# Kernel optimization log

Hardware: AMD Instinct MI355X
Metric: run time of the kernel (lower is better)

## Reference

```python
import jax, jax.numpy as jnp
import numpy as np

B, S, T, C, H = 16, 64, 4096, 512, 8
D = C // H
NEG = jnp.float32(-1e30)


def setup_inputs() -> dict:
    key = jax.random.key(0)
    ks = jax.random.split(key, 12)
    x = jax.random.normal(ks[0], (1, C, 1), dtype=jnp.float32)
    eh = jax.random.normal(ks[1], (B, C, T), dtype=jnp.float32)
    # ragged shot boundaries -> fixed (B, S) start/end arrays, end > start
    bounds = jnp.sort(jax.random.randint(ks[2], (B, S + 1), 0, T), axis=-1)
    shot_starts = bounds[:, :-1].astype(jnp.int32)
    shot_ends = jnp.maximum(bounds[:, 1:], shot_starts + 1).astype(jnp.int32)
    sc = 1.0 / np.sqrt(C)
    Wq = jax.random.normal(ks[3], (C, C), dtype=jnp.float32) * sc
    bq = jnp.zeros((C,), dtype=jnp.float32)
    Wk = jax.random.normal(ks[4], (C, C), dtype=jnp.float32) * sc
    bk = jnp.zeros((C,), dtype=jnp.float32)
    Wv = jax.random.normal(ks[5], (C, C), dtype=jnp.float32) * sc
    bv = jnp.zeros((C,), dtype=jnp.float32)
    Wp = jax.random.normal(ks[6], (C, C), dtype=jnp.float32) * sc
    bp = jnp.zeros((C,), dtype=jnp.float32)
    return {"x": x, "encoder_hidden_states": eh, "shot_starts": shot_starts,
            "shot_ends": shot_ends, "Wq": Wq, "bq": bq, "Wk": Wk, "bk": bk,
            "Wv": Wv, "bv": bv, "Wp": Wp, "bp": bp}


def reference(x, encoder_hidden_states, shot_starts, shot_ends,
              Wq, bq, Wk, bk, Wv, bv, Wp, bp):
    scale = 1.0 / np.sqrt(D)
    # 1x1 conv == pointwise matmul over channels
    q = (Wq @ x[0] + bq[:, None])            # (C, 1)
    k = jnp.einsum('oc,bct->bot', Wk, encoder_hidden_states) + bk[None, :, None]
    v = jnp.einsum('oc,bct->bot', Wv, encoder_hidden_states) + bv[None, :, None]
    qh = q.reshape(H, D) * scale             # (H, D) single query per head
    kh = k.reshape(B, H, D, T)               # (B, H, D, T)
    vh = v.reshape(B, H, D, T).transpose(0, 1, 3, 2)  # (B, H, T, D)
    att = jnp.einsum('hd,bhdt->bht', qh, kh)          # (B, H, T)
    pos = jnp.arange(T)
    seg = (pos[None, None, :] >= shot_starts[:, :, None]) & \
          (pos[None, None, :] < shot_ends[:, :, None])  # (B, S, T)
    logits = jnp.where(seg[:, :, None, :], att[:, None, :, :], NEG)  # (B,S,H,T)
    p = jax.nn.softmax(logits, axis=-1)
    out = jnp.einsum('bsht,bhtd->bshd', p, vh)        # (B, S, H, D)
    out = out.reshape(B * S, C)
    out = out @ Wp.T + bp                              # proj (1x1 conv)
    return out[:, :, None]                             # (B*S, C, 1)
```

## Files before the change

### kernel.cpp

```cpp
#include <hip/hip_runtime.h>
#include <cstdint>
#include <cstddef>

#define B_ 16
#define S_ 64
#define T_ 4096
#define C_ 512
#define H_ 8

#define WS_QKT     0
#define WS_QB      4096
#define WS_QH      4104
#define WS_MS      4616
#define WS_LI      12808
#define WS_CNT     21000
#define WS_CSEG    21016
#define WS_CIDX    23064
#define WS_CMUL    25112
#define WS_ATT     28672
#define WS_WSUM    552960
#define WS_ATTNOUT 4747264

__global__ void k_prep1(const float* __restrict__ x, const float* __restrict__ Wq,
                        const float* __restrict__ bq, float* __restrict__ qh_g) {
  __shared__ float xs[C_];
  __shared__ float red[256];
  int tid = threadIdx.x;
  xs[tid] = x[tid];
  xs[tid + 256] = x[tid + 256];
  __syncthreads();
  int r0 = blockIdx.x * 32;
  int rl = tid >> 3, sub = tid & 7;
  int r = r0 + rl;
  const float* wr = Wq + (size_t)r * C_ + sub * 64;
  const float* xp = xs + sub * 64;
  float s = 0.f;
#pragma unroll
  for (int i = 0; i < 64; i += 4) {
    float4 w = *(const float4*)(wr + i);
    s += w.x * xp[i] + w.y * xp[i + 1] + w.z * xp[i + 2] + w.w * xp[i + 3];
  }
  red[tid] = s;
  __syncthreads();
  if (sub == 0) {
    float tot = bq[r];
#pragma unroll
    for (int i = 0; i < 8; ++i) tot += red[rl * 8 + i];
    qh_g[r] = tot * 0.125f;
  }
}

__global__ void k_prep2(const float* __restrict__ qh_g,
                        const float* __restrict__ Wk,
                        const float* __restrict__ bk, float* __restrict__ qkT,
                        float* __restrict__ qb) {
  __shared__ float qhs[64];
  int tid = threadIdx.x;
  int h = blockIdx.x;
  if (tid < 64) qhs[tid] = qh_g[h * 64 + tid];
  __syncthreads();
  int c0 = tid, c1 = tid + 256;
  float s0 = 0.f, s1 = 0.f;
#pragma unroll 8
  for (int d = 0; d < 64; ++d) {
    const float* row = Wk + (size_t)(h * 64 + d) * C_;
    float q = qhs[d];
    s0 += q * row[c0];
    s1 += q * row[c1];
  }
  qkT[c0 * 8 + h] = s0;
  qkT[c1 * 8 + h] = s1;
  if (tid < 64) {
    float w = qhs[tid] * bk[h * 64 + tid];
#pragma unroll
    for (int off = 32; off > 0; off >>= 1) w += __shfl_down(w, off, 64);
    if (tid == 0) qb[h] = w;
  }
}

__global__ __launch_bounds__(256, 4) void k_att(
    const float* __restrict__ eh, const float* __restrict__ qkT,
    const float* __restrict__ qb, float* __restrict__ att) {
  __shared__ float qks[C_ * 8];
  __shared__ float part[4 * 8 * 64];
  int tid = threadIdx.x;
  int tl = tid & 63, cg = tid >> 6;
  int b = blockIdx.y;
  int t0 = blockIdx.x * 64;
#pragma unroll
  for (int i = 0; i < 16; ++i) qks[tid + i * 256] = qkT[tid + i * 256];
  __syncthreads();
  const float* ehp = eh + ((size_t)b * C_ + (size_t)cg * 128) * T_ + t0 + tl;
  float acc[8];
#pragma unroll
  for (int h = 0; h < 8; ++h) acc[h] = 0.f;
#pragma unroll 4
  for (int j = 0; j < 128; ++j) {
    float e = ehp[(size_t)j * T_];
    const float4 q0 = *(const float4*)&qks[(cg * 128 + j) * 8];
    const float4 q1 = *(const float4*)&qks[(cg * 128 + j) * 8 + 4];
    acc[0] += q0.x * e; acc[1] += q0.y * e; acc[2] += q0.z * e; acc[3] += q0.w * e;
    acc[4] += q1.x * e; acc[5] += q1.y * e; acc[6] += q1.z * e; acc[7] += q1.w * e;
  }
#pragma unroll
  for (int h = 0; h < 8; ++h) part[(cg * 8 + h) * 64 + tl] = acc[h];
  __syncthreads();
#pragma unroll
  for (int i = 0; i < 2; ++i) {
    int idx = tid + i * 256;
    int h = idx >> 6, tt = idx & 63;
    float v = part[(0 * 8 + h) * 64 + tt] + part[(1 * 8 + h) * 64 + tt] +
              part[(2 * 8 + h) * 64 + tt] + part[(3 * 8 + h) * 64 + tt] + qb[h];
    att[((size_t)b * H_ + h) * T_ + t0 + tt] = v;
  }
}

__global__ void k_stats(const float* __restrict__ att,
                        const int* __restrict__ starts,
                        const int* __restrict__ ends, float* __restrict__ ms,
                        float* __restrict__ li) {
  int tid = threadIdx.x;
  int n = blockIdx.x;
  int b = n >> 6;
  int start = starts[n], end = ends[n];
  int h = tid >> 5, tl = tid & 31;
  const float* ah = att + ((size_t)b * H_ + h) * T_;
  float mloc = -3.0e38f;
  for (int t = start + tl; t < end; t += 32) mloc = fmaxf(mloc, ah[t]);
#pragma unroll
  for (int off = 16; off > 0; off >>= 1)
    mloc = fmaxf(mloc, __shfl_xor(mloc, off, 32));
  float lloc = 0.f;
  for (int t = start + tl; t < end; t += 32) lloc += __expf(ah[t] - mloc);
#pragma unroll
  for (int off = 16; off > 0; off >>= 1) lloc += __shfl_xor(lloc, off, 32);
  if (tl == 0) { ms[n * 8 + h] = mloc; li[n * 8 + h] = 1.f / lloc; }
}

__global__ void k_map(const int* __restrict__ starts,
                      const int* __restrict__ ends, int* __restrict__ cnt,
                      int* __restrict__ cseg, int* __restrict__ cidx,
                      int* __restrict__ cmul) {
  __shared__ int sc[1024];
  int n = threadIdx.x;
  int st = starts[n], en = ends[n];
  int cbase = st & ~31;
  int nch = (en - cbase + 127) >> 7;
  sc[n] = nch;
  __syncthreads();
  for (int off = 1; off < 1024; off <<= 1) {
    int v = 0;
    if (n >= off) v = sc[n - off];
    __syncthreads();
    sc[n] += v;
    __syncthreads();
  }
  int pre = sc[n] - nch;
  for (int k = 0; k < nch; ++k) {
    cseg[pre + k] = n;
    cidx[pre + k] = k;
    cmul[pre + k] = (nch > 1) ? 1 : 0;
  }
  if (n == 1023) cnt[0] = sc[n];
}

__global__ __launch_bounds__(256, 4) void k_wsum(
    const float* __restrict__ eh, const float* __restrict__ att,
    const float* __restrict__ ms, const float* __restrict__ li,
    const int* __restrict__ starts, const int* __restrict__ ends,
    const int* __restrict__ cnt, const int* __restrict__ cseg,
    const int* __restrict__ cidx, const int* __restrict__ cmul,
    float* __restrict__ wsum) {
  __shared__ float pl[8 * 136];
  int i = blockIdx.x;
  if (i >= cnt[0]) return;
  int tid = threadIdx.x;
  int n = cseg[i];
  int k = cidx[i];
  int mul = cmul[i];
  int b = n >> 6;
  int st = starts[n], en = ends[n];
  int cbase = st & ~31;
  int t_lo = cbase + k * 128;
  if (st > t_lo) t_lo = st;
  int t_hi = cbase + (k + 1) * 128;
  if (en < t_hi) t_hi = en;
  int base = t_lo & ~3;

  int h = tid >> 5, l32 = tid & 31;
  float msn = ms[n * 8 + h], lin = li[n * 8 + h];
  const float* ah = att + ((size_t)b * H_ + h) * T_;
  for (int j = l32; j < 136; j += 32) {
    int t = base + j;
    float pv = 0.f;
    if (t >= t_lo && t < t_hi) pv = __expf(ah[t] - msn) * lin;
    pl[h * 136 + j] = pv;
  }
  __syncthreads();

  float acc0[8], acc1[8];
#pragma unroll
  for (int hh = 0; hh < 8; ++hh) { acc0[hh] = 0.f; acc1[hh] = 0.f; }
  const float* e0p = eh + ((size_t)b * C_ + tid) * T_ + base;
  const float* e1p = e0p + (size_t)256 * T_;
  int jmax = t_hi - base;
  int jv = jmax & ~3;
#pragma unroll 4
  for (int j = 0; j < jv; j += 4) {
    float4 e0 = *(const float4*)(e0p + j);
    float4 e1 = *(const float4*)(e1p + j);
#pragma unroll
    for (int hh = 0; hh < 8; ++hh) {
      const float4 p = *(const float4*)&pl[hh * 136 + j];
      acc0[hh] += p.x * e0.x + p.y * e0.y + p.z * e0.z + p.w * e0.w;
      acc1[hh] += p.x * e1.x + p.y * e1.y + p.z * e1.z + p.w * e1.w;
    }
  }
  for (int j = jv; j < jmax; ++j) {
    float e0 = e0p[j], e1 = e1p[j];
#pragma unroll
    for (int hh = 0; hh < 8; ++hh) {
      float p = pl[hh * 136 + j];
      acc0[hh] += p * e0;
      acc1[hh] += p * e1;
    }
  }
  float* wp = wsum + (size_t)n * (H_ * C_);
  if (!mul) {
#pragma unroll
    for (int hh = 0; hh < 8; ++hh) {
      wp[hh * C_ + tid] = acc0[hh];
      wp[hh * C_ + 256 + tid] = acc1[hh];
    }
  } else {
#pragma unroll
    for (int hh = 0; hh < 8; ++hh) {
      atomicAdd(&wp[hh * C_ + tid], acc0[hh]);
      atomicAdd(&wp[hh * C_ + 256 + tid], acc1[hh]);
    }
  }
}

__global__ __launch_bounds__(256, 4) void k_gemm(
    const float* __restrict__ A, long aRow, long aColPerY,
    const float* __restrict__ Bm, const float* __restrict__ bias,
    float* __restrict__ Cc) {
  __shared__ float As[32 * 36];
  __shared__ float Bs[64 * 36];
  int tid = threadIdx.x;
  int n0 = blockIdx.x * 32;
  int y = blockIdx.y;
  const float* Abase = A + (size_t)n0 * aRow + (size_t)y * aColPerY;
  const float* Bbase = Bm + (size_t)(y * 64) * C_;
  int tx = tid & 15, ty = tid >> 4;
  float acc[2][4];
#pragma unroll
  for (int a = 0; a < 2; ++a)
#pragma unroll
    for (int bb = 0; bb < 4; ++bb) acc[a][bb] = 0.f;
  for (int k0 = 0; k0 < 512; k0 += 32) {
#pragma unroll
    for (int i = 0; i < 4; ++i) {
      int idx = tid + i * 256;
      int r = idx >> 5, cc = idx & 31;
      As[r * 36 + cc] = Abase[(size_t)r * aRow + k0 + cc];
    }
#pragma unroll
    for (int i = 0; i < 8; ++i) {
      int idx = tid + i * 256;
      int r = idx >> 5, cc = idx & 31;
      Bs[r * 36 + cc] = Bbase[(size_t)r * C_ + k0 + cc];
    }
    __syncthreads();
#pragma unroll
    for (int k = 0; k < 32; k += 4) {
      const float4 a0 = *(const float4*)&As[(ty * 2 + 0) * 36 + k];
      const float4 a1 = *(const float4*)&As[(ty * 2 + 1) * 36 + k];
#pragma unroll
      for (int bb = 0; bb < 4; ++bb) {
        const float4 bv = *(const float4*)&Bs[(tx * 4 + bb) * 36 + k];
        acc[0][bb] += a0.x * bv.x + a0.y * bv.y + a0.z * bv.z + a0.w * bv.w;
        acc[1][bb] += a1.x * bv.x + a1.y * bv.y + a1.z * bv.z + a1.w * bv.w;
      }
    }
    __syncthreads();
  }
#pragma unroll
  for (int a = 0; a < 2; ++a) {
    int nn = n0 + ty * 2 + a;
    float4 o;
    o.x = acc[a][0] + bias[y * 64 + tx * 4 + 0];
    o.y = acc[a][1] + bias[y * 64 + tx * 4 + 1];
    o.z = acc[a][2] + bias[y * 64 + tx * 4 + 2];
    o.w = acc[a][3] + bias[y * 64 + tx * 4 + 3];
    *(float4*)&Cc[(size_t)nn * C_ + y * 64 + tx * 4] = o;
  }
}

extern "C" void kernel_launch(void* const* d_in, const int* in_sizes, int n_in,
                              void* d_out, int out_size, void* d_ws,
                              size_t ws_size, hipStream_t stream) {
  const float* x = (const float*)d_in[0];
  const float* eh = (const float*)d_in[1];
  const int* shot_starts = (const int*)d_in[2];
  const int* shot_ends = (const int*)d_in[3];
  const float* Wq = (const float*)d_in[4];
  const float* bq = (const float*)d_in[5];
  const float* Wk = (const float*)d_in[6];
  const float* bk = (const float*)d_in[7];
  const float* Wv = (const float*)d_in[8];
  const float* bv = (const float*)d_in[9];
  const float* Wp = (const float*)d_in[10];
  const float* bp = (const float*)d_in[11];
  float* out = (float*)d_out;

  float* ws = (float*)d_ws;
  float* qkT = ws + WS_QKT;
  float* qb = ws + WS_QB;
  float* qh = ws + WS_QH;
  float* ms = ws + WS_MS;
  float* li = ws + WS_LI;
  int* cnt = (int*)(ws + WS_CNT);
  int* cseg = (int*)(ws + WS_CSEG);
  int* cidx = (int*)(ws + WS_CIDX);
  int* cmul = (int*)(ws + WS_CMUL);
  float* att = ws + WS_ATT;
  float* wsum = ws + WS_WSUM;
  float* attnout = ws + WS_ATTNOUT;

  hipMemsetAsync(wsum, 0, (size_t)1024 * H_ * C_ * sizeof(float), stream);
  k_prep1<<<16, 256, 0, stream>>>(x, Wq, bq, qh);
  k_prep2<<<8, 256, 0, stream>>>(qh, Wk, bk, qkT, qb);
  k_att<<<dim3(T_ / 64, B_), 256, 0, stream>>>(eh, qkT, qb, att);
  k_stats<<<B_ * S_, 256, 0, stream>>>(att, shot_starts, shot_ends, ms, li);
  k_map<<<1, 1024, 0, stream>>>(shot_starts, shot_ends, cnt, cseg, cidx, cmul);
  k_wsum<<<2048, 256, 0, stream>>>(eh, att, ms, li, shot_starts, shot_ends,
                                   cnt, cseg, cidx, cmul, wsum);
  k_gemm<<<dim3(32, 8), 256, 0, stream>>>(wsum, (long)(H_ * C_), (long)C_, Wv,
                                          bv, attnout);
  k_gemm<<<dim3(32, 8), 256, 0, stream>>>(attnout, (long)C_, 0L, Wp, bp, out);
}
```

Baseline: 367.4 us.

## Restructure weighted-sum kernel so lane groups cover contiguous time chunks per channel

The weighted-sum kernel used to give each thread one channel pair and walk time serially, so every lane read a different row with a large stride. Now each group of 4 lanes shares a channel and reads 64 contiguous bytes of time per step. Partial sums are combined with shuffles, and the kernel makes 8 passes over 64 channels. Chunk alignment moves from 32 to 16 elements to cut wasted work at segment edges. The cost is extra shuffle reductions, loads clamped near the end of the row, and more passes per block.

Measured after the change: 347.4 us. 1.06x faster.

```diff
diff --git a/kernel.cpp b/kernel.cpp
--- a/kernel.cpp
+++ b/kernel.cpp
@@ -144,7 +144,7 @@
   __shared__ int sc[1024];
   int n = threadIdx.x;
   int st = starts[n], en = ends[n];
-  int cbase = st & ~31;
+  int cbase = st & ~15;
   int nch = (en - cbase + 127) >> 7;
   sc[n] = nch;
   __syncthreads();
@@ -180,63 +180,78 @@
   int mul = cmul[i];
   int b = n >> 6;
   int st = starts[n], en = ends[n];
-  int cbase = st & ~31;
-  int t_lo = cbase + k * 128;
-  if (st > t_lo) t_lo = st;
-  int t_hi = cbase + (k + 1) * 128;
+  int cbase = st & ~15;
+  int base = cbase + (k << 7);
+  int t_lo = (st > base) ? st : base;
+  int t_hi = base + 128;
   if (en < t_hi) t_hi = en;
-  int base = t_lo & ~3;
-
-  int h = tid >> 5, l32 = tid & 31;
-  float msn = ms[n * 8 + h], lin = li[n * 8 + h];
-  const float* ah = att + ((size_t)b * H_ + h) * T_;
-  for (int j = l32; j < 136; j += 32) {
-    int t = base + j;
-    float pv = 0.f;
-    if (t >= t_lo && t < t_hi) pv = __expf(ah[t] - msn) * lin;
-    pl[h * 136 + j] = pv;
-  }
-  __syncthreads();
-
-  float acc0[8], acc1[8];
-#pragma unroll
-  for (int hh = 0; hh < 8; ++hh) { acc0[hh] = 0.f; acc1[hh] = 0.f; }
-  const float* e0p = eh + ((size_t)b * C_ + tid) * T_ + base;
-  const float* e1p = e0p + (size_t)256 * T_;
   int jmax = t_hi - base;
-  int jv = jmax & ~3;
-#pragma unroll 4
-  for (int j = 0; j < jv; j += 4) {
-    float4 e0 = *(const float4*)(e0p + j);
-    float4 e1 = *(const float4*)(e1p + j);
-#pragma unroll
-    for (int hh = 0; hh < 8; ++hh) {
-      const float4 p = *(const float4*)&pl[hh * 136 + j];
-      acc0[hh] += p.x * e0.x + p.y * e0.y + p.z * e0.z + p.w * e0.w;
-      acc1[hh] += p.x * e1.x + p.y * e1.y + p.z * e1.z + p.w * e1.w;
-    }
-  }
-  for (int j = jv; j < jmax; ++j) {
-    float e0 = e0p[j], e1 = e1p[j];
-#pragma unroll
-    for (int hh = 0; hh < 8; ++hh) {
-      float p = pl[hh * 136 + j];
-      acc0[hh] += p * e0;
-      acc1[hh] += p * e1;
-    }
-  }
+  int kmax = (jmax + 15) >> 4;
+
+  {
+    int h = tid >> 5, l32 = tid & 31;
+    float msn = ms[n * 8 + h], lin = li[n * 8 + h];
+    const float* ah = att + ((size_t)b * H_ + h) * T_;
+    for (int j = l32; j < 136; j += 32) {
+      int t = base + j;
+      float pv = 0.f;
+      if (t >= t_lo && t < t_hi) pv = __expf(ah[t] - msn) * lin;
+      pl[h * 136 + j] = pv;
+    }
+  }
+  __syncthreads();
+
+  int l = tid & 63, wv = tid >> 6;
+  int il = l & 3, g = l >> 2;
   float* wp = wsum + (size_t)n * (H_ * C_);
-  if (!mul) {
-#pragma unroll
-    for (int hh = 0; hh < 8; ++hh) {
-      wp[hh * C_ + tid] = acc0[hh];
-      wp[hh * C_ + 256 + tid] = acc1[hh];
-    }
-  } else {
-#pragma unroll
-    for (int hh = 0; hh < 8; ++hh) {
-      atomicAdd(&wp[hh * C_ + tid], acc0[hh]);
-      atomicAdd(&wp[hh * C_ + 256 + tid], acc1[hh]);
+
+  for (int pass = 0; pass < 8; ++pass) {
+    int ch = pass * 64 + wv * 16 + g;
+    const float* erow = eh + ((size_t)b * C_ + ch) * T_;
+    float a0 = 0.f, a1 = 0.f, a2 = 0.f, a3 = 0.f;
+    float a4 = 0.f, a5 = 0.f, a6 = 0.f, a7 = 0.f;
+#pragma unroll 2
+    for (int kk = 0; kk < kmax; ++kk) {
+      int j0 = (kk << 4) | (il << 2);
+      int tg = base + j0;
+      if (tg > T_ - 4) tg = T_ - 4;
+      float4 ev = *(const float4*)(erow + tg);
+      const float* pp = pl + j0;
+      float4 p;
+      p = *(const float4*)(pp + 0 * 136);
+      a0 += p.x * ev.x + p.y * ev.y + p.z * ev.z + p.w * ev.w;
+      p = *(const float4*)(pp + 1 * 136);
+      a1 += p.x * ev.x + p.y * ev.y + p.z * ev.z + p.w * ev.w;
+      p = *(const float4*)(pp + 2 * 136);
+      a2 += p.x * ev.x + p.y * ev.y + p.z * ev.z + p.w * ev.w;
+      p = *(const float4*)(pp + 3 * 136);
+      a3 += p.x * ev.x + p.y * ev.y + p.z * ev.z + p.w * ev.w;
+      p = *(const float4*)(pp + 4 * 136);
+      a4 += p.x * ev.x + p.y * ev.y + p.z * ev.z + p.w * ev.w;
+      p = *(const float4*)(pp + 5 * 136);
+      a5 += p.x * ev.x + p.y * ev.y + p.z * ev.z + p.w * ev.w;
+      p = *(const float4*)(pp + 6 * 136);
+      a6 += p.x * ev.x + p.y * ev.y + p.z * ev.z + p.w * ev.w;
+      p = *(const float4*)(pp + 7 * 136);
+      a7 += p.x * ev.x + p.y * ev.y + p.z * ev.z + p.w * ev.w;
+    }
+    a0 += __shfl_xor(a0, 1); a0 += __shfl_xor(a0, 2);
+    a1 += __shfl_xor(a1, 1); a1 += __shfl_xor(a1, 2);
+    a2 += __shfl_xor(a2, 1); a2 += __shfl_xor(a2, 2);
+    a3 += __shfl_xor(a3, 1); a3 += __shfl_xor(a3, 2);
+    a4 += __shfl_xor(a4, 1); a4 += __shfl_xor(a4, 2);
+    a5 += __shfl_xor(a5, 1); a5 += __shfl_xor(a5, 2);
+    a6 += __shfl_xor(a6, 1); a6 += __shfl_xor(a6, 2);
+    a7 += __shfl_xor(a7, 1); a7 += __shfl_xor(a7, 2);
+    float s0 = (il < 2) ? ((il == 0) ? a0 : a2) : ((il == 2) ? a4 : a6);
+    float s1 = (il < 2) ? ((il == 0) ? a1 : a3) : ((il == 2) ? a5 : a7);
+    int h0 = il << 1;
+    if (!mul) {
+      wp[h0 * C_ + ch] = s0;
+      wp[(h0 + 1) * C_ + ch] = s1;
+    } else {
+      atomicAdd(&wp[h0 * C_ + ch], s0);
+      atomicAdd(&wp[(h0 + 1) * C_ + ch], s1);
     }
   }
 }
```
